# Optimization experiments

Measured on AMD Instinct MI355X. Metric: run time of the kernel, lower is better.

Reference implementation:

```python
import jax, jax.numpy as jnp
import numpy as np

T = 100  # number of time steps
B = 256
F = 4096

def setup_inputs() -> dict:
    key = jax.random.key(0)
    k1, k2 = jax.random.split(key)
    x = jax.random.uniform(k1, (B, F), dtype=jnp.float32)
    delays = jax.random.uniform(k2, (F,), dtype=jnp.float32)
    return {"x": x, "delays": delays}

def reference(x, delays):
    # spike_times: [B, F] int, truncation toward zero like torch .long()
    st = ((1.0 - x * delays[None, :]) * (T - 1)).astype(jnp.int32)
    st = jnp.clip(st, 0, T - 1)
    # one-hot over time axis -> [B, T, F]
    t_axis = jnp.arange(T, dtype=jnp.int32)[None, :, None]  # [1, T, 1]
    spikes = (t_axis == st[:, None, :]).astype(jnp.float32)
    return spikes
```

## Files before the change

kernel.cpp:

```cpp
#include <hip/hip_runtime.h>

constexpr int T  = 100;
constexpr int B  = 256;
constexpr int F  = 4096;
constexpr int F4 = F / 4;

typedef float        floatx4 __attribute__((ext_vector_type(4)));
typedef unsigned int u32;
typedef u32          u32x4   __attribute__((ext_vector_type(4)));

__global__ __launch_bounds__(256) void build_st(
    const float* __restrict__ x,
    const float* __restrict__ delays,
    u32* __restrict__ stw)
{
    const int idx = blockIdx.x * 256 + threadIdx.x;
    const int f4  = idx & (F4 - 1);

    const floatx4 xv = reinterpret_cast<const floatx4*>(x)[idx];
    const floatx4 dv = reinterpret_cast<const floatx4*>(delays)[f4];

    auto sti = [](float xi, float di) -> u32 {
        float p  = __fmul_rn(xi, di);
        float s  = __fsub_rn(1.0f, p);
        float v  = __fmul_rn(s, 99.0f);
        int   st = (int)v;
        st = st < 0 ? 0 : st;
        st = st > (T - 1) ? (T - 1) : st;
        return (u32)st;
    };

    const u32 w = sti(xv.x, dv.x)
                | (sti(xv.y, dv.y) << 8)
                | (sti(xv.z, dv.z) << 16)
                | (sti(xv.w, dv.w) << 24);
    stw[idx] = w;
}

__global__ __launch_bounds__(256) void scatter_lines(
    const u32* __restrict__ stw,
    float* __restrict__ out)
{
    const int idx = blockIdx.x * 256 + threadIdx.x;
    const int f4  = idx & (F4 - 1);
    const int b   = idx >> 10;
    const int L   = f4 >> 2;

    const u32   w  = stw[idx];
    const u32x4 tw = reinterpret_cast<const u32x4*>(stw)[idx >> 2];

    const int st0 =  w        & 255u;
    const int st1 = (w >> 8)  & 255u;
    const int st2 = (w >> 16) & 255u;
    const int st3 =  w >> 24;

    floatx4* base = reinterpret_cast<floatx4*>(out)
                  + ((size_t)b * T) * F4 + (L << 2);

    auto write_line = [&](int t) {
        floatx4* lp = base + (size_t)t * F4;
#pragma unroll
        for (int g = 0; g < 4; ++g) {
            const u32 tg = tw[g];
            floatx4 v;
            v.x = ((int)( tg        & 255u) == t) ? 1.0f : 0.0f;
            v.y = ((int)((tg >> 8)  & 255u) == t) ? 1.0f : 0.0f;
            v.z = ((int)((tg >> 16) & 255u) == t) ? 1.0f : 0.0f;
            v.w = ((int)( tg >> 24        ) == t) ? 1.0f : 0.0f;
            lp[g] = v;
        }
    };

    write_line(st0);
    if (st1 != st0)                             write_line(st1);
    if (st2 != st0 && st2 != st1)               write_line(st2);
    if (st3 != st0 && st3 != st1 && st3 != st2) write_line(st3);
}

__global__ __launch_bounds__(256) void spike_kernel_fb(
    const float* __restrict__ x,
    const float* __restrict__ delays,
    float* __restrict__ out)
{
    const int idx = blockIdx.x * blockDim.x + threadIdx.x;
    const int f4  = idx & (F4 - 1);
    const int b   = idx >> 10;

    const floatx4 xv = reinterpret_cast<const floatx4*>(x)[idx];
    const floatx4 dv = reinterpret_cast<const floatx4*>(delays)[f4];

    auto spike_time = [](float xi, float di) -> int {
        float p  = __fmul_rn(xi, di);
        float s  = __fsub_rn(1.0f, p);
        float v  = __fmul_rn(s, 99.0f);
        int   st = (int)v;
        st = st < 0 ? 0 : st;
        st = st > (T - 1) ? (T - 1) : st;
        return st;
    };
    const int st0 = spike_time(xv.x, dv.x);
    const int st1 = spike_time(xv.y, dv.y);
    const int st2 = spike_time(xv.z, dv.z);
    const int st3 = spike_time(xv.w, dv.w);

    floatx4* outp = reinterpret_cast<floatx4*>(out) + (size_t)b * T * F4 + f4;
#pragma unroll 4
    for (int t = 0; t < T; ++t) {
        floatx4 v;
        v.x = (t == st0) ? 1.0f : 0.0f;
        v.y = (t == st1) ? 1.0f : 0.0f;
        v.z = (t == st2) ? 1.0f : 0.0f;
        v.w = (t == st3) ? 1.0f : 0.0f;
        outp[(size_t)t * F4] = v;
    }
}

extern "C" void kernel_launch(void* const* d_in, const int* in_sizes, int n_in,
                              void* d_out, int out_size, void* d_ws, size_t ws_size,
                              hipStream_t stream)
{
    const float* x      = reinterpret_cast<const float*>(d_in[0]);
    const float* delays = reinterpret_cast<const float*>(d_in[1]);
    float* out          = reinterpret_cast<float*>(d_out);

    const size_t needed = (size_t)B * F4 * sizeof(u32);
    if (ws_size >= needed && d_ws != nullptr) {
        u32* stw = reinterpret_cast<u32*>(d_ws);
        build_st<<<B * F4 / 256, 256, 0, stream>>>(x, delays, stw);
        hipMemsetAsync(out, 0, (size_t)out_size, stream);
        scatter_lines<<<B * F4 / 256, 256, 0, stream>>>(stw, out);
    } else {
        spike_kernel_fb<<<B * F4 / 256, 256, 0, stream>>>(x, delays, out);
    }
}
```

Baseline: 394.9 us.

## Remap scatter to one thread per 16-feature line with bitmask dedup

```diff
diff --git a/kernel.cpp b/kernel.cpp
--- a/kernel.cpp
+++ b/kernel.cpp
@@ -4,10 +4,12 @@
 constexpr int B  = 256;
 constexpr int F  = 4096;
 constexpr int F4 = F / 4;
+constexpr int NL = F / 16;
 
-typedef float        floatx4 __attribute__((ext_vector_type(4)));
-typedef unsigned int u32;
-typedef u32          u32x4   __attribute__((ext_vector_type(4)));
+typedef float         floatx4 __attribute__((ext_vector_type(4)));
+typedef unsigned int  u32;
+typedef unsigned long long u64;
+typedef u32           u32x4   __attribute__((ext_vector_type(4)));
 
 __global__ __launch_bounds__(256) void build_st(
     const float* __restrict__ x,
@@ -41,40 +43,44 @@
     const u32* __restrict__ stw,
     float* __restrict__ out)
 {
-    const int idx = blockIdx.x * 256 + threadIdx.x;
-    const int f4  = idx & (F4 - 1);
-    const int b   = idx >> 10;
-    const int L   = f4 >> 2;
+    const int L  = threadIdx.x;
+    const int b  = blockIdx.x >> 1;
+    const int t0 = (blockIdx.x & 1) * 50;
 
-    const u32   w  = stw[idx];
-    const u32x4 tw = reinterpret_cast<const u32x4*>(stw)[idx >> 2];
+    const u32x4 tw = reinterpret_cast<const u32x4*>(stw)[b * NL + L];
 
-    const int st0 =  w        & 255u;
-    const int st1 = (w >> 8)  & 255u;
-    const int st2 = (w >> 16) & 255u;
-    const int st3 =  w >> 24;
+    u64 mlo = 0, mhi = 0;
+#pragma unroll
+    for (int g = 0; g < 4; ++g) {
+        const u32 tg = tw[g];
+#pragma unroll
+        for (int k = 0; k < 4; ++k) {
+            const u32 t8 = (tg >> (8 * k)) & 255u;
+            if (t8 < 64u) mlo |= 1ull << t8;
+            else          mhi |= 1ull << (t8 - 64u);
+        }
+    }
 
     floatx4* base = reinterpret_cast<floatx4*>(out)
-                  + ((size_t)b * T) * F4 + (L << 2);
+                  + (size_t)b * T * F4 + (L << 2);
 
-    auto write_line = [&](int t) {
-        floatx4* lp = base + (size_t)t * F4;
+    for (int t = t0; t < t0 + 50; ++t) {
+        const bool present = (t < 64) ? ((mlo >> t) & 1ull)
+                                      : ((mhi >> (t - 64)) & 1ull);
+        if (present) {
+            floatx4* lp = base + (size_t)t * F4;
 #pragma unroll
-        for (int g = 0; g < 4; ++g) {
-            const u32 tg = tw[g];
-            floatx4 v;
-            v.x = ((int)( tg        & 255u) == t) ? 1.0f : 0.0f;
-            v.y = ((int)((tg >> 8)  & 255u) == t) ? 1.0f : 0.0f;
-            v.z = ((int)((tg >> 16) & 255u) == t) ? 1.0f : 0.0f;
-            v.w = ((int)( tg >> 24        ) == t) ? 1.0f : 0.0f;
-            lp[g] = v;
+            for (int g = 0; g < 4; ++g) {
+                const u32 tg = tw[g];
+                floatx4 v;
+                v.x = ((int)( tg        & 255u) == t) ? 1.0f : 0.0f;
+                v.y = ((int)((tg >> 8)  & 255u) == t) ? 1.0f : 0.0f;
+                v.z = ((int)((tg >> 16) & 255u) == t) ? 1.0f : 0.0f;
+                v.w = ((int)( tg >> 24        ) == t) ? 1.0f : 0.0f;
+                lp[g] = v;
+            }
         }
-    };
-
-    write_line(st0);
-    if (st1 != st0)                             write_line(st1);
-    if (st2 != st0 && st2 != st1)               write_line(st2);
-    if (st3 != st0 && st3 != st1 && st3 != st2) write_line(st3);
+    }
 }
 
 __global__ __launch_bounds__(256) void spike_kernel_fb(
@@ -128,7 +134,7 @@
         u32* stw = reinterpret_cast<u32*>(d_ws);
         build_st<<<B * F4 / 256, 256, 0, stream>>>(x, delays, stw);
         hipMemsetAsync(out, 0, (size_t)out_size, stream);
-        scatter_lines<<<B * F4 / 256, 256, 0, stream>>>(stw, out);
+        scatter_lines<<<B * 2, 256, 0, stream>>>(stw, out);
     } else {
         spike_kernel_fb<<<B * F4 / 256, 256, 0, stream>>>(x, delays, out);
     }
```

After: 404.8 us. 2.5% more time.
